# Kernel optimization log

Measured on AMD Instinct MI355X. Metric: run time of the kernel, lower is better.

## Reference

```python
import jax, jax.numpy as jnp
import numpy as np

B, T, D = 2, 2048, 2048
N, K, H = 16, 8, 128  # num_heads, num_kv_heads, head_dim
SOFTCAP = 50.0
ROPE_BASE = 10000.0


def apply_rope(x, positions):
    # x: [B, L, heads, H], positions: [B, L]
    head_dim = x.shape[-1]
    fraction = 2.0 * jnp.arange(head_dim // 2, dtype=jnp.float32) / head_dim
    timescale = ROPE_BASE ** fraction  # [H/2]
    sinusoid = positions.astype(jnp.float32)[..., None] / timescale  # [B, L, H/2]
    sinusoid = sinusoid[..., None, :]  # [B, L, 1, H/2]
    sin, cos = jnp.sin(sinusoid), jnp.cos(sinusoid)
    first, second = jnp.split(x, 2, axis=-1)
    out = jnp.concatenate([first * cos - second * sin,
                           second * cos + first * sin], axis=-1)
    return out.astype(x.dtype)


def setup_inputs() -> dict:
    key = jax.random.key(0)
    kx, kq, kkv, ko = jax.random.split(key, 4)
    x = jax.random.normal(kx, (B, T, D), dtype=jnp.float32)
    positions = jnp.broadcast_to(jnp.arange(T, dtype=jnp.int32), (B, T))
    attn_mask = jnp.broadcast_to(
        jnp.tril(jnp.ones((T, T), dtype=bool))[None, None], (B, 1, T, T))
    # variance-scaling fan_in init approximated with scaled normals
    w_q = jax.random.normal(kq, (N, D, H), dtype=jnp.float32) / np.sqrt(D)
    w_kv = jax.random.normal(kkv, (2, K, D, H), dtype=jnp.float32) / np.sqrt(D)
    w_out = jax.random.normal(ko, (N, H, D), dtype=jnp.float32) / np.sqrt(N * H)
    return {"x": x, "positions": positions, "attn_mask": attn_mask,
            "w_q": w_q, "w_kv": w_kv, "w_out": w_out}


def reference(x, positions, attn_mask, w_q, w_kv, w_out):
    # QKV projections (GQA: separate q and kv einsums)
    q = jnp.einsum('BTD,NDH->BTNH', x, w_q)        # [B,T,N,H]
    kv = jnp.einsum('BSD,cKDH->cBSKH', x, w_kv)     # [2,B,S,K,H]
    k, v = kv[0], kv[1]
    q = apply_rope(q, positions) * (H ** -0.5)      # rsqrt_head_dim norm
    k = apply_rope(k, positions)
    # GQA grouping: N = K * G
    G = N // K
    qg = q.reshape(B, T, K, G, H)
    logits = jnp.einsum('BTKGH,BSKH->BKGTS', qg, k).astype(jnp.float32)
    logits = jnp.tanh(logits / SOFTCAP) * SOFTCAP   # logits softcap
    big_neg = -2.3819763e+38
    masked = jnp.where(attn_mask[:, :, None, :, :], logits, big_neg)
    probs = jax.nn.softmax(masked, axis=-1).astype(k.dtype)
    encoded = jnp.einsum('BKGTS,BSKH->BTKGH', probs, v).reshape(B, T, N, H)
    return jnp.einsum('BTNH,NHD->BTD', encoded, w_out)
```

## Files before the change

kernel.cpp:

```cpp
#include <hip/hip_runtime.h>
#include <math.h>
#include <stdint.h>


typedef unsigned short u16;
using bf16x8 = __attribute__((ext_vector_type(8))) short;
using f32x4  = __attribute__((ext_vector_type(4))) float;

#define MFMA_BF16(a,b,c) __builtin_amdgcn_mfma_f32_16x16x32_bf16((a),(b),(c),0,0,0)

static __device__ __forceinline__ float b2f(u16 u) {
  union { unsigned int i; float f; } v; v.i = ((unsigned int)u) << 16; return v.f;
}
static __device__ __forceinline__ u16 f2b(float f) {
  union { float f; unsigned int i; } v; v.f = f;
  unsigned int r = v.i + 0x7fffu + ((v.i >> 16) & 1u);
  return (u16)(r >> 16);
}
static __device__ __forceinline__ unsigned pk2(float x0, float x1) {
  union { float f; unsigned u; } a, b;
  a.f = x0; b.f = x1;
  return __builtin_amdgcn_perm(b.u + 0x8000u, a.u + 0x8000u, 0x07060302u);
}
static __device__ __forceinline__ void gload_lds16(const void* g, void* l) {
  __builtin_amdgcn_global_load_lds((__attribute__((address_space(1))) void*)(g),
                                   (__attribute__((address_space(3))) void*)(l),
                                   16, 0, 0);
}

__global__ __launch_bounds__(256) void prep(const float* __restrict__ x, u16* __restrict__ xb,
                                            const float* __restrict__ wq,
                                            const float* __restrict__ wkv,
                                            const float* __restrict__ wout,
                                            u16* __restrict__ wqkvt, u16* __restrict__ woutt) {
  const int tid = threadIdx.x;
  int bid = blockIdx.x;
  if (bid < 8192) {
    const int i = (bid * 256 + tid) * 4;
    const float4 v = *(const float4*)(x + i);
    ushort4 o;
    o.x = f2b(v.x); o.y = f2b(v.y); o.z = f2b(v.z); o.w = f2b(v.w);
    *(ushort4*)(xb + i) = o;
    return;
  }
  bid -= 8192;
  const float* src;
  u16* dst;
  int rows, cols, bx, by;
  if (bid < 8192) {
    const int seg = bid >> 12;
    const int r = bid & 4095;
    const int mat = r >> 8;
    bx = (r & 255) & 3;
    by = (r & 255) >> 2;
    rows = 2048; cols = 128;
    src = (seg ? wkv : wq) + (size_t)mat * 2048 * 128;
    dst = wqkvt + (size_t)(seg * 16 + mat) * 2048 * 128;
  } else {
    const int r = bid - 8192;
    bx = r & 63;
    by = r >> 6;
    rows = 2048; cols = 2048;
    src = wout;
    dst = woutt;
  }
  __shared__ u16 tile[32][33];
  const int c0 = bx * 32, r0 = by * 32;
  const int tx = tid & 31, ty = tid >> 5;
#pragma unroll
  for (int j = 0; j < 4; ++j)
    tile[ty + j * 8][tx] = f2b(src[(size_t)(r0 + ty + j * 8) * cols + (c0 + tx)]);
  __syncthreads();
#pragma unroll
  for (int j = 0; j < 4; ++j)
    dst[(size_t)(c0 + ty + j * 8) * rows + (r0 + tx)] = tile[tx][ty + j * 8];
}

__global__ __launch_bounds__(512, 2) void gemm_qkv(const u16* __restrict__ X,
                                                   const u16* __restrict__ wqkvt,
                                                   u16* __restrict__ qb,
                                                   u16* __restrict__ kb,
                                                   u16* __restrict__ vtb) {
  __shared__ __align__(16) u16 sAB[2][2][16384];
  const int m0 = blockIdx.x * 256;
  const int ct0 = blockIdx.y * 2;
  const u16* BT = wqkvt + (size_t)blockIdx.y * 256 * 2048;
  const int tid = threadIdx.x;
  const int wave = tid >> 6, lane = tid & 63;
  const int wm = wave >> 2, wn = wave & 3;
  const int quad = lane >> 4, l16 = lane & 15;
  const int srow = lane >> 3;
  const int sch = (lane & 7) ^ srow;

  f32x4 acc[8][4] = {};

  auto STAGE = [&](int kt, int bsel) {
    const int k0 = kt * 64;
#pragma unroll
    for (int s = 0; s < 4; ++s) {
      const int ia = wave * 4 + s;
      const int row = ia * 8 + srow;
      gload_lds16(X + (size_t)(m0 + row) * 2048 + k0 + sch * 8,
                  (char*)&sAB[bsel][0][0] + ia * 1024);
      gload_lds16(BT + (size_t)row * 2048 + k0 + sch * 8,
                  (char*)&sAB[bsel][1][0] + ia * 1024);
    }
  };

  auto COMPUTE = [&](int bsel) {
    const char* aB = (const char*)&sAB[bsel][0][0];
    const char* bB = (const char*)&sAB[bsel][1][0];
#pragma unroll
    for (int ks = 0; ks < 2; ++ks) {
      bf16x8 bfr[4];
#pragma unroll
      for (int nf = 0; nf < 4; ++nf) {
        const int Rb = wn * 64 + nf * 16 + l16;
        bfr[nf] = *(const bf16x8*)(bB + Rb * 128 + (((ks * 4 + quad) ^ (Rb & 7)) << 4));
      }
      __builtin_amdgcn_s_setprio(1);
#pragma unroll
      for (int mf = 0; mf < 8; ++mf) {
        const int R = wm * 128 + mf * 16 + l16;
        const bf16x8 af = *(const bf16x8*)(aB + R * 128 + (((ks * 4 + quad) ^ (R & 7)) << 4));
#pragma unroll
        for (int nf = 0; nf < 4; ++nf)
          acc[mf][nf] = MFMA_BF16(af, bfr[nf], acc[mf][nf]);
      }
      __builtin_amdgcn_s_setprio(0);
    }
  };

  STAGE(0, 0);
#pragma unroll 1
  for (int t = 0; t < 31; ++t) {
    STAGE(t + 1, (t + 1) & 1);
    asm volatile("s_waitcnt vmcnt(8)" ::: "memory");
    __builtin_amdgcn_s_barrier();
    asm volatile("" ::: "memory");
    COMPUTE(t & 1);
    asm volatile("" ::: "memory");
    __builtin_amdgcn_s_barrier();
    asm volatile("" ::: "memory");
  }
  asm volatile("s_waitcnt vmcnt(0)" ::: "memory");
  __builtin_amdgcn_s_barrier();
  asm volatile("" ::: "memory");
  COMPUTE(1);

#pragma unroll
  for (int mf = 0; mf < 8; ++mf) {
    const int mm = m0 + wm * 128 + mf * 16 + quad * 4;
    const int b = mm >> 11;
    const int t = mm & 2047;
#pragma unroll
    for (int nf = 0; nf < 4; ++nf) {
      const int colg = wn * 64 + nf * 16;
      const int ct = ct0 + (colg >> 7);
      const int h = (colg & 127) + l16;
      if (ct < 16) {
        u16* d = qb + (((size_t)b * 16 + ct) * 2048 + t) * 128 + h;
#pragma unroll
        for (int i = 0; i < 4; ++i) d[(size_t)i * 128] = f2b(acc[mf][nf][i]);
      } else if (ct < 24) {
        u16* d = kb + (((size_t)b * 8 + (ct - 16)) * 2048 + t) * 128 + h;
#pragma unroll
        for (int i = 0; i < 4; ++i) d[(size_t)i * 128] = f2b(acc[mf][nf][i]);
      } else {
        u16* d = vtb + (((size_t)b * 8 + (ct - 24)) * 128 + h) * 2048 + t;
        uint2 pkv;
        pkv.x = (unsigned)f2b(acc[mf][nf][0]) | ((unsigned)f2b(acc[mf][nf][1]) << 16);
        pkv.y = (unsigned)f2b(acc[mf][nf][2]) | ((unsigned)f2b(acc[mf][nf][3]) << 16);
        *(uint2*)d = pkv;
      }
    }
  }
}

__global__ __launch_bounds__(256) void rope_kernel(u16* __restrict__ qb,
                                                   u16* __restrict__ kb,
                                                   const int* __restrict__ pos) {
  const unsigned idx = blockIdx.x * 256 + threadIdx.x;
  const unsigned QP = 1u << 21;
  u16* p;
  float scale;
  int b, t, j2;
  if (idx < QP) {
    j2 = (int)(idx & 31) * 2; t = (int)((idx >> 5) & 2047);
    const int hd = (int)((idx >> 16) & 15); b = (int)(idx >> 20);
    p = qb + (((size_t)b * 16 + hd) * 2048 + t) * 128;
    scale = 0.08838834764831845f;
  } else {
    const unsigned r = idx - QP;
    j2 = (int)(r & 31) * 2; t = (int)((r >> 5) & 2047);
    const int hd = (int)((r >> 16) & 7); b = (int)(r >> 19);
    p = kb + (((size_t)b * 8 + hd) * 2048 + t) * 128;
    scale = 1.0f;
  }
  const float fpos = (float)pos[(size_t)b * 2048 + t];
  const unsigned lo = *(const unsigned*)(p + j2);
  const unsigned hi = *(const unsigned*)(p + j2 + 64);
  unsigned olo = 0, ohi = 0;
#pragma unroll
  for (int d = 0; d < 2; ++d) {
    const int j = j2 + d;
    const float ts = __powf(10000.0f, (float)j * (1.0f / 64.0f));
    float sn, cs;
    sincosf(fpos / ts, &sn, &cs);
    const float a = b2f((u16)((d ? (lo >> 16) : lo) & 0xffffu));
    const float c2 = b2f((u16)((d ? (hi >> 16) : hi) & 0xffffu));
    olo |= ((unsigned)f2b((a * cs - c2 * sn) * scale)) << (16 * d);
    ohi |= ((unsigned)f2b((c2 * cs + a * sn) * scale)) << (16 * d);
  }
  *(unsigned*)(p + j2) = olo;
  *(unsigned*)(p + j2 + 64) = ohi;
}

__global__ __launch_bounds__(256, 4) void attn_fused(const u16* __restrict__ qg,
                                                     const u16* __restrict__ kg,
                                                     const u16* __restrict__ vtg,
                                                     u16* __restrict__ enc) {
  __shared__ __align__(16) char lds[32768];
  char* sK = lds;
  char* sV = lds + 16384;

  const int bid = blockIdx.x;
  const int half = bid >> 9;
  const int r = bid & 511;
  const int x = r & 7;
  const int g = r >> 3;
  const int pr = g & 15;
  const int head = (g >> 4) * 8 + x;
  const int Q = half ? pr : (31 - pr);
  const int b = head >> 4;
  const int n = head & 15;
  const int kh = n >> 1;

  const u16* qbase = qg + ((size_t)b * 16 + n) * 2048 * 128;
  const u16* kbase = kg + ((size_t)b * 8 + kh) * 2048 * 128;
  const u16* vbase = vtg + ((size_t)b * 8 + kh) * 128 * 2048;

  const int tid = threadIdx.x, wave = tid >> 6, lane = tid & 63;
  const int quad = lane >> 4, l16 = lane & 15;
  const int bp_a0 = ((quad & 1) * 32 + l16) * 4;
  const int bp_a1 = bp_a0 + 64;

  const float L2E = 1.4426950408889634f;
  const float C50 = 72.13475204444817f;
  const float A1 = 1.3333333333e-4f;
  const float A2 = 2.1333333333e-8f;
  const float A3 = 3.4539682540e-12f;

  const u16* kp[4];
  const u16* vp[4];
#pragma unroll
  for (int s = 0; s < 4; ++s) {
    const int kr = wave * 16 + s * 4 + quad;
    kp[s] = kbase + (size_t)kr * 128 + (l16 ^ (s * 4 + quad)) * 8;
    const int vr = wave * 32 + s * 8 + (lane >> 3);
    vp[s] = vbase + (size_t)vr * 2048 + ((lane & 7) ^ (lane >> 3)) * 8;
  }

  const int tw = Q * 64 + wave * 16;
  const int tlane = tw + l16;

  bf16x8 qf[4];
#pragma unroll
  for (int kf = 0; kf < 4; ++kf)
    qf[kf] = *(const bf16x8*)(qbase + (size_t)tlane * 128 + kf * 32 + quad * 8);

  f32x4 o[8] = {};
  f32x4 lacc = {0.f, 0.f, 0.f, 0.f};

#pragma unroll 1
  for (int si = 0; si <= Q; ++si) {
    const int s0 = si * 64;
    __syncthreads();
#pragma unroll
    for (int s = 0; s < 4; ++s) {
      gload_lds16(kp[s], sK + (wave * 4 + s) * 1024);
      gload_lds16(vp[s], sV + (wave * 4 + s) * 1024);
      kp[s] += 64 * 128;
      vp[s] += 64;
    }
    __syncthreads();

    const bool diag = (si == Q);
    const int nfmax = diag ? wave : 3;
    const int kmax = diag ? (wave >> 1) : 1;

    f32x4 sacc[4];
#pragma unroll
    for (int nf = 0; nf < 4; ++nf) {
      if (nf <= nfmax) {
        const int sr = nf * 16 + l16;
        f32x4 a = {0.f, 0.f, 0.f, 0.f};
#pragma unroll
        for (int kf = 0; kf < 4; ++kf) {
          const bf16x8 kfr =
              *(const bf16x8*)(sK + sr * 256 + (((kf * 4 + quad) ^ (sr & 15)) << 4));
          a = MFMA_BF16(kfr, qf[kf], a);
        }
        sacc[nf] = a;
      }
    }

#pragma unroll
    for (int nf = 0; nf < 4; ++nf) {
      if (nf <= nfmax) {
        const f32x4 xv = sacc[nf];
        const f32x4 u = xv * xv;
        f32x4 t = u * (-A3) + A2;
        t = u * t + (-A1);
        t = u * t + 1.0f;
        const f32x4 tc = xv * t;
        f32x4 pv;
#pragma unroll
        for (int i = 0; i < 4; ++i) pv[i] = exp2f(fmaf(tc[i], L2E, -C50));
        if (diag) {
#pragma unroll
          for (int i = 0; i < 4; ++i) {
            const int sg = s0 + nf * 16 + quad * 4 + i;
            if (sg > tlane) pv[i] = 0.0f;
          }
        }
        sacc[nf] = pv;
        lacc += pv;
      }
    }

    unsigned pkd[4][2];
#pragma unroll
    for (int nf = 0; nf < 4; ++nf) {
      if (nf <= nfmax) {
        pkd[nf][0] = pk2(sacc[nf][0], sacc[nf][1]);
        pkd[nf][1] = pk2(sacc[nf][2], sacc[nf][3]);
      } else {
        pkd[nf][0] = 0u; pkd[nf][1] = 0u;
      }
    }

#pragma unroll
    for (int c2 = 0; c2 < 2; ++c2) {
      if (c2 <= kmax) {
        const int lo = (quad >> 1);
        const int dA0 = __builtin_amdgcn_ds_bpermute(bp_a0, (int)pkd[2 * c2][0]);
        const int dB0 = __builtin_amdgcn_ds_bpermute(bp_a0, (int)pkd[2 * c2 + 1][0]);
        const int dA1 = __builtin_amdgcn_ds_bpermute(bp_a0, (int)pkd[2 * c2][1]);
        const int dB1 = __builtin_amdgcn_ds_bpermute(bp_a0, (int)pkd[2 * c2 + 1][1]);
        const int dA2 = __builtin_amdgcn_ds_bpermute(bp_a1, (int)pkd[2 * c2][0]);
        const int dB2 = __builtin_amdgcn_ds_bpermute(bp_a1, (int)pkd[2 * c2 + 1][0]);
        const int dA3 = __builtin_amdgcn_ds_bpermute(bp_a1, (int)pkd[2 * c2][1]);
        const int dB3 = __builtin_amdgcn_ds_bpermute(bp_a1, (int)pkd[2 * c2 + 1][1]);
        union { int d[4]; bf16x8 v; } pb;
        pb.d[0] = lo ? dB0 : dA0;
        pb.d[1] = lo ? dB1 : dA1;
        pb.d[2] = lo ? dB2 : dA2;
        pb.d[3] = lo ? dB3 : dA3;
#pragma unroll
        for (int nfo = 0; nfo < 8; ++nfo) {
          const int hr = nfo * 16 + l16;
          const bf16x8 vb =
              *(const bf16x8*)(sV + hr * 128 + (((c2 * 4 + quad) ^ (hr & 7)) << 4));
          o[nfo] = MFMA_BF16(vb, pb.v, o[nfo]);
        }
      }
    }
  }

  float lsum = lacc[0] + lacc[1] + lacc[2] + lacc[3];
  lsum += __shfl_xor(lsum, 16);
  lsum += __shfl_xor(lsum, 32);
  const float inv = 1.0f / lsum;
  u16* d = enc + (((size_t)b * 2048 + tlane) * 16 + n) * 128 + quad * 4;
#pragma unroll
  for (int nfo = 0; nfo < 8; ++nfo) {
    uint2 st;
    st.x = (unsigned)f2b(o[nfo][0] * inv) | ((unsigned)f2b(o[nfo][1] * inv) << 16);
    st.y = (unsigned)f2b(o[nfo][2] * inv) | ((unsigned)f2b(o[nfo][3] * inv) << 16);
    *(uint2*)(d + nfo * 16) = st;
  }
}

__global__ __launch_bounds__(256) void gemm_out(const u16* __restrict__ A,
                                                const u16* __restrict__ Bt,
                                                float* __restrict__ C) {
  __shared__ __align__(16) u16 sA[128 * 64];
  __shared__ __align__(16) u16 sB[128 * 64];
  const int m0 = blockIdx.x * 128;
  const int n0 = blockIdx.y * 128;
  const int tid = threadIdx.x;
  const int wave = tid >> 6, lane = tid & 63;
  const int wm = wave & 1, wn = wave >> 1;
  const int quad = lane >> 4, l16 = lane & 15;
  const int srow = lane >> 3;
  const int sch = (lane & 7) ^ srow;

  f32x4 acc[4][4] = {};

  for (int k0 = 0; k0 < 2048; k0 += 64) {
#pragma unroll
    for (int s = 0; s < 4; ++s) {
      const int instr = wave * 4 + s;
      const int row = instr * 8 + srow;
      gload_lds16(A + (size_t)(m0 + row) * 2048 + k0 + sch * 8, (char*)sA + instr * 1024);
      gload_lds16(Bt + (size_t)(n0 + row) * 2048 + k0 + sch * 8, (char*)sB + instr * 1024);
    }
    __syncthreads();
#pragma unroll
    for (int ks = 0; ks < 2; ++ks) {
      bf16x8 af[4], bfr[4];
#pragma unroll
      for (int mf = 0; mf < 4; ++mf) {
        const int R = wm * 64 + mf * 16 + l16;
        af[mf] = *(const bf16x8*)((char*)sA + R * 128 + (((ks * 4 + quad) ^ (R & 7)) << 4));
      }
#pragma unroll
      for (int nf = 0; nf < 4; ++nf) {
        const int R = wn * 64 + nf * 16 + l16;
        bfr[nf] = *(const bf16x8*)((char*)sB + R * 128 + (((ks * 4 + quad) ^ (R & 7)) << 4));
      }
#pragma unroll
      for (int mf = 0; mf < 4; ++mf)
#pragma unroll
        for (int nf = 0; nf < 4; ++nf)
          acc[mf][nf] = MFMA_BF16(af[mf], bfr[nf], acc[mf][nf]);
    }
    __syncthreads();
  }

#pragma unroll
  for (int mf = 0; mf < 4; ++mf) {
    const int mm = m0 + wm * 64 + mf * 16 + quad * 4;
#pragma unroll
    for (int nf = 0; nf < 4; ++nf) {
      const int col = n0 + wn * 64 + nf * 16 + l16;
#pragma unroll
      for (int i = 0; i < 4; ++i) C[(size_t)(mm + i) * 2048 + col] = acc[mf][nf][i];
    }
  }
}

extern "C" void kernel_launch(void* const* d_in, const int* in_sizes, int n_in,
                              void* d_out, int out_size, void* d_ws, size_t ws_size,
                              hipStream_t stream) {
  (void)in_sizes; (void)n_in; (void)out_size; (void)ws_size;
  const float* x     = (const float*)d_in[0];
  const int*   posi  = (const int*)d_in[1];
  const float* w_q   = (const float*)d_in[3];
  const float* w_kv  = (const float*)d_in[4];
  const float* w_out = (const float*)d_in[5];
  float* out = (float*)d_out;

  u16* ws = (u16*)d_ws;
  u16* wqkvt = ws;
  u16* woutt = ws + (size_t)8388608;
  u16* qb    = ws + (size_t)12582912;
  u16* kb    = ws + (size_t)20971520;
  u16* vtb   = ws + (size_t)25165824;
  u16* encb  = ws + (size_t)29360128;
  u16* xb    = encb;

  prep<<<20480, 256, 0, stream>>>(x, xb, w_q, w_kv, w_out, wqkvt, woutt);
  gemm_qkv<<<dim3(16, 16), 512, 0, stream>>>(xb, wqkvt, qb, kb, vtb);
  rope_kernel<<<12288, 256, 0, stream>>>(qb, kb, posi);
  attn_fused<<<1024, 256, 0, stream>>>(qb, kb, vtb, encb);
  gemm_out<<<dim3(32, 16), 256, 0, stream>>>(encb, woutt, out);
}
```

Measured before the change: 361.1 us.

## Double-buffer LDS in attention and output GEMM with prefetch of next tile

The attention kernel now keeps two LDS stages and issues the next K/V tile's global-to-LDS loads before computing on the current one. It waits with a partial vmcnt instead of two full syncthreads per iteration. The output GEMM is reworked into 256x128 tiles with 512 threads, the same double-buffered prefetch pipeline and s_setprio around the MFMA bursts. The goal is to hide global load latency behind MFMA work, at the cost of doubled LDS use: the attention launch bound drops from 4 to 2 blocks per CU, which lowers occupancy.

```diff
diff --git a/kernel.cpp b/kernel.cpp
--- a/kernel.cpp
+++ b/kernel.cpp
@@ -216,13 +216,11 @@
   *(unsigned*)(p + j2 + 64) = ohi;
 }
 
-__global__ __launch_bounds__(256, 4) void attn_fused(const u16* __restrict__ qg,
+__global__ __launch_bounds__(256, 2) void attn_fused(const u16* __restrict__ qg,
                                                      const u16* __restrict__ kg,
                                                      const u16* __restrict__ vtg,
                                                      u16* __restrict__ enc) {
-  __shared__ __align__(16) char lds[32768];
-  char* sK = lds;
-  char* sV = lds + 16384;
+  __shared__ __align__(16) char lds[2][32768];
 
   const int bid = blockIdx.x;
   const int half = bid >> 9;
@@ -261,6 +259,17 @@
     vp[s] = vbase + (size_t)vr * 2048 + ((lane & 7) ^ (lane >> 3)) * 8;
   }
 
+  auto STAGE = [&](int bsel) {
+    char* base = &lds[bsel][0];
+#pragma unroll
+    for (int s = 0; s < 4; ++s) {
+      gload_lds16(kp[s], base + (wave * 4 + s) * 1024);
+      gload_lds16(vp[s], base + 16384 + (wave * 4 + s) * 1024);
+      kp[s] += 64 * 128;
+      vp[s] += 64;
+    }
+  };
+
   const int tw = Q * 64 + wave * 16;
   const int tlane = tw + l16;
 
@@ -271,19 +280,23 @@
 
   f32x4 o[8] = {};
   f32x4 lacc = {0.f, 0.f, 0.f, 0.f};
+
+  STAGE(0);
 
 #pragma unroll 1
   for (int si = 0; si <= Q; ++si) {
     const int s0 = si * 64;
-    __syncthreads();
-#pragma unroll
-    for (int s = 0; s < 4; ++s) {
-      gload_lds16(kp[s], sK + (wave * 4 + s) * 1024);
-      gload_lds16(vp[s], sV + (wave * 4 + s) * 1024);
-      kp[s] += 64 * 128;
-      vp[s] += 64;
-    }
-    __syncthreads();
+    if (si < Q) {
+      STAGE((si + 1) & 1);
+      asm volatile("s_waitcnt vmcnt(8)" ::: "memory");
+    } else {
+      asm volatile("s_waitcnt vmcnt(0)" ::: "memory");
+    }
+    __builtin_amdgcn_s_barrier();
+    asm volatile("" ::: "memory");
+
+    const char* sK = &lds[si & 1][0];
+    const char* sV = &lds[si & 1][0] + 16384;
 
     const bool diag = (si == Q);
     const int nfmax = diag ? wave : 3;
@@ -366,6 +379,9 @@
         }
       }
     }
+    asm volatile("" ::: "memory");
+    __builtin_amdgcn_s_barrier();
+    asm volatile("" ::: "memory");
   }
 
   float lsum = lacc[0] + lacc[1] + lacc[2] + lacc[3];
@@ -382,59 +398,87 @@
   }
 }
 
-__global__ __launch_bounds__(256) void gemm_out(const u16* __restrict__ A,
-                                                const u16* __restrict__ Bt,
-                                                float* __restrict__ C) {
-  __shared__ __align__(16) u16 sA[128 * 64];
-  __shared__ __align__(16) u16 sB[128 * 64];
-  const int m0 = blockIdx.x * 128;
+__global__ __launch_bounds__(512, 2) void gemm_out(const u16* __restrict__ A,
+                                                   const u16* __restrict__ Bt,
+                                                   float* __restrict__ C) {
+  __shared__ __align__(16) u16 sA[2][16384];
+  __shared__ __align__(16) u16 sB[2][8192];
+  const int m0 = blockIdx.x * 256;
   const int n0 = blockIdx.y * 128;
   const int tid = threadIdx.x;
   const int wave = tid >> 6, lane = tid & 63;
-  const int wm = wave & 1, wn = wave >> 1;
+  const int wm = wave >> 2, wn = wave & 3;
   const int quad = lane >> 4, l16 = lane & 15;
   const int srow = lane >> 3;
   const int sch = (lane & 7) ^ srow;
 
-  f32x4 acc[4][4] = {};
-
-  for (int k0 = 0; k0 < 2048; k0 += 64) {
+  f32x4 acc[8][2] = {};
+
+  auto STAGE = [&](int kt, int bsel) {
+    const int k0 = kt * 64;
 #pragma unroll
     for (int s = 0; s < 4; ++s) {
-      const int instr = wave * 4 + s;
-      const int row = instr * 8 + srow;
-      gload_lds16(A + (size_t)(m0 + row) * 2048 + k0 + sch * 8, (char*)sA + instr * 1024);
-      gload_lds16(Bt + (size_t)(n0 + row) * 2048 + k0 + sch * 8, (char*)sB + instr * 1024);
-    }
-    __syncthreads();
+      const int ia = wave * 4 + s;
+      const int row = ia * 8 + srow;
+      gload_lds16(A + (size_t)(m0 + row) * 2048 + k0 + sch * 8,
+                  (char*)&sA[bsel][0] + ia * 1024);
+    }
+#pragma unroll
+    for (int s = 0; s < 2; ++s) {
+      const int ib = wave * 2 + s;
+      const int row = ib * 8 + srow;
+      gload_lds16(Bt + (size_t)(n0 + row) * 2048 + k0 + sch * 8,
+                  (char*)&sB[bsel][0] + ib * 1024);
+    }
+  };
+
+  auto COMPUTE = [&](int bsel) {
+    const char* aB = (const char*)&sA[bsel][0];
+    const char* bB = (const char*)&sB[bsel][0];
 #pragma unroll
     for (int ks = 0; ks < 2; ++ks) {
-      bf16x8 af[4], bfr[4];
-#pragma unroll
-      for (int mf = 0; mf < 4; ++mf) {
-        const int R = wm * 64 + mf * 16 + l16;
-        af[mf] = *(const bf16x8*)((char*)sA + R * 128 + (((ks * 4 + quad) ^ (R & 7)) << 4));
-      }
-#pragma unroll
-      for (int nf = 0; nf < 4; ++nf) {
-        const int R = wn * 64 + nf * 16 + l16;
-        bfr[nf] = *(const bf16x8*)((char*)sB + R * 128 + (((ks * 4 + quad) ^ (R & 7)) << 4));
-      }
-#pragma unroll
-      for (int mf = 0; mf < 4; ++mf)
-#pragma unroll
-        for (int nf = 0; nf < 4; ++nf)
-          acc[mf][nf] = MFMA_BF16(af[mf], bfr[nf], acc[mf][nf]);
-    }
-    __syncthreads();
-  }
-
-#pragma unroll
-  for (int mf = 0; mf < 4; ++mf) {
-    const int mm = m0 + wm * 64 + mf * 16 + quad * 4;
-#pragma unroll
-    for (int nf = 0; nf < 4; ++nf) {
-      const int col = n0 + wn * 64 + nf * 16 + l16;
+      bf16x8 bfr[2];
+#pragma unroll
+      for (int nf = 0; nf < 2; ++nf) {
+        const int Rb = wn * 32 + nf * 16 + l16;
+        bfr[nf] = *(const bf16x8*)(bB + Rb * 128 + (((ks * 4 + quad) ^ (Rb & 7)) << 4));
+      }
+      __builtin_amdgcn_s_setprio(1);
+#pragma unroll
+      for (int mf = 0; mf < 8; ++mf) {
+        const int R = wm * 128 + mf * 16 + l16;
+        const bf16x8 af = *(const bf16x8*)(aB + R * 128 + (((ks * 4 + quad) ^ (R & 7)) << 4));
+#pragma unroll
+        for (int nf = 0; nf < 2; ++nf)
+          acc[mf][nf] = MFMA_BF16(af, bfr[nf], acc[mf][nf]);
+      }
+      __builtin_amdgcn_s_setprio(0);
+    }
+  };
+
+  STAGE(0, 0);
+#pragma unroll 1
+  for (int t = 0; t < 31; ++t) {
+    STAGE(t + 1, (t + 1) & 1);
+    asm volatile("s_waitcnt vmcnt(6)" ::: "memory");
+    __builtin_amdgcn_s_barrier();
+    asm volatile("" ::: "memory");
+    COMPUTE(t & 1);
+    asm volatile("" ::: "memory");
+    __builtin_amdgcn_s_barrier();
+    asm volatile("" ::: "memory");
+  }
+  asm volatile("s_waitcnt vmcnt(0)" ::: "memory");
+  __builtin_amdgcn_s_barrier();
+  asm volatile("" ::: "memory");
+  COMPUTE(1);
+
+#pragma unroll
+  for (int mf = 0; mf < 8; ++mf) {
+    const int mm = m0 + wm * 128 + mf * 16 + quad * 4;
+#pragma unroll
+    for (int nf = 0; nf < 2; ++nf) {
+      const int col = n0 + wn * 32 + nf * 16 + l16;
 #pragma unroll
       for (int i = 0; i < 4; ++i) C[(size_t)(mm + i) * 2048 + col] = acc[mf][nf][i];
     }
@@ -465,5 +509,5 @@
   gemm_qkv<<<dim3(16, 16), 512, 0, stream>>>(xb, wqkvt, qb, kb, vtb);
   rope_kernel<<<12288, 256, 0, stream>>>(qb, kb, posi);
   attn_fused<<<1024, 256, 0, stream>>>(qb, kb, vtb, encb);
-  gemm_out<<<dim3(32, 16), 256, 0, stream>>>(encb, woutt, out);
-}
+  gemm_out<<<dim3(16, 16), 512, 0, stream>>>(encb, woutt, out);
+}
```

New measurement: 386.3 us. +7.0%, slower.
